# Optimization experiments

Measured on AMD Instinct MI355X. Metric: run time of the kernel, lower is better.

Reference implementation:

```python
import jax, jax.numpy as jnp
import numpy as np

N_E = 1024
E_DIM = 256
GAMMA = 0.1
TEMPERATURE = 0.1


def setup_inputs() -> dict:
    key = jax.random.key(0)
    k1, k2 = jax.random.split(key)
    z = jax.random.normal(k1, (64, 512, E_DIM), dtype=jnp.float32)
    # embedding initialized uniform(-1/n_e, 1/n_e) as in the torch module
    emb = jax.random.uniform(k2, (N_E, E_DIM), dtype=jnp.float32,
                             minval=-1.0 / N_E, maxval=1.0 / N_E)
    return {"z": z, "emb": emb}


def reference(z, emb):
    # z: [B, S, D] -> flatten to [N, D]
    zf = z.reshape(-1, E_DIM)
    # squared euclidean distance via sum-of-squares + matmul: [N, n_e]
    d = (jnp.sum(zf * zf, axis=1, keepdims=True)
         + jnp.sum(emb * emb, axis=1)
         - 2.0 * jnp.einsum('nd,ed->ne', zf, emb))
    exp_d = jnp.exp(-d / GAMMA)
    # soft assignment weights (note: softmax of exp(-d/gamma)/temperature,
    # exactly as in the original module)
    w = jax.nn.softmax(exp_d / TEMPERATURE, axis=-1)
    return w
```

## Files before the change

kernel.cpp:

```cpp
#include <hip/hip_runtime.h>

#define NTOK 32768
#define NE   1024
#define DD   256

typedef __attribute__((ext_vector_type(4))) float f32x4;

__global__ __launch_bounds__(256) void prep_norm_kernel(
    const float* __restrict__ emb, float* __restrict__ pmax)
{
    __shared__ float sm[4];
    const int w = threadIdx.x >> 6;
    const int l = threadIdx.x & 63;
    float m = 0.f;
#pragma unroll
    for (int k = 0; k < 4; ++k) {
        const int row = blockIdx.x * 16 + w * 4 + k;
        f32x4 v = *(const f32x4*)(emb + (size_t)row * DD + l * 4);
        float ss = v.x * v.x + v.y * v.y + v.z * v.z + v.w * v.w;
#pragma unroll
        for (int off = 32; off; off >>= 1) ss += __shfl_xor(ss, off, 64);
        m = fmaxf(m, ss);
    }
    if (l == 0) sm[w] = m;
    __syncthreads();
    if (threadIdx.x == 0)
        pmax[blockIdx.x] = fmaxf(fmaxf(sm[0], sm[1]), fmaxf(sm[2], sm[3]));
}

__device__ __attribute__((noinline)) void slow_row(
    const float* __restrict__ emb, float* __restrict__ out,
    int row, float ss, f32x4 v, int l)
{
    const int c0 = l * 16;
    float acc[16];
    float s = 0.f;
#pragma unroll
    for (int ch = 0; ch < 4; ++ch) {
        float dot[4] = {0.f, 0.f, 0.f, 0.f};
        float ene[4] = {0.f, 0.f, 0.f, 0.f};
        for (int d4 = 0; d4 < 64; ++d4) {
            f32x4 zz;
            zz.x = __shfl(v.x, d4); zz.y = __shfl(v.y, d4);
            zz.z = __shfl(v.z, d4); zz.w = __shfl(v.w, d4);
#pragma unroll
            for (int c = 0; c < 4; ++c) {
                f32x4 ev = *(const f32x4*)(emb + (size_t)(c0 + ch * 4 + c) * DD + d4 * 4);
                dot[c] = fmaf(zz.x, ev.x, fmaf(zz.y, ev.y,
                         fmaf(zz.z, ev.z, fmaf(zz.w, ev.w, dot[c]))));
                ene[c] = fmaf(ev.x, ev.x, fmaf(ev.y, ev.y,
                         fmaf(ev.z, ev.z, fmaf(ev.w, ev.w, ene[c]))));
            }
        }
#pragma unroll
        for (int c = 0; c < 4; ++c) {
            const float d = ss + ene[c] - 2.0f * dot[c];
            const float u = 10.0f * expf(-10.0f * d);
            const float e = expf(u);
            acc[ch * 4 + c] = e;
            s += e;
        }
    }
#pragma unroll
    for (int off = 32; off; off >>= 1) s += __shfl_xor(s, off, 64);
    const float inv = 1.0f / s;
#pragma unroll
    for (int ch = 0; ch < 4; ++ch) {
        f32x4 o = { acc[ch * 4] * inv, acc[ch * 4 + 1] * inv,
                    acc[ch * 4 + 2] * inv, acc[ch * 4 + 3] * inv };
        *(f32x4*)(out + (size_t)row * NE + c0 + ch * 4) = o;
    }
}

__global__ __launch_bounds__(256, 8) void sq_main_kernel(
    const float* __restrict__ z, const float* __restrict__ emb,
    const float* __restrict__ pmax, float* __restrict__ out)
{
    const int w  = threadIdx.x >> 6;
    const int l  = threadIdx.x & 63;
    const int r0 = (blockIdx.x * 4 + w) * 2;

    f32x4 v0 = *(const f32x4*)(z + (size_t)r0 * DD + l * 4);
    f32x4 v1 = *(const f32x4*)(z + (size_t)(r0 + 1) * DD + l * 4);

    float m = pmax[l];
#pragma unroll
    for (int off = 32; off; off >>= 1) m = fmaxf(m, __shfl_xor(m, off, 64));
    const float E   = sqrtf(m);
    const float rhs = (3.0f + E) * (3.0f + E);

    float s0 = v0.x * v0.x + v0.y * v0.y + v0.z * v0.z + v0.w * v0.w;
    float s1 = v1.x * v1.x + v1.y * v1.y + v1.z * v1.z + v1.w * v1.w;
#pragma unroll
    for (int off = 32; off; off >>= 1) {
        s0 += __shfl_xor(s0, off, 64);
        s1 += __shfl_xor(s1, off, 64);
    }

    const float c = 0.0009765625f;
    const f32x4 cv = {c, c, c, c};
    if (s0 >= rhs) {
        float* ob = out + (size_t)r0 * NE + l * 4;
#pragma unroll
        for (int i = 0; i < 4; ++i) *(f32x4*)(ob + i * 256) = cv;
    } else {
        slow_row(emb, out, r0, s0, v0, l);
    }
    if (s1 >= rhs) {
        float* ob = out + (size_t)(r0 + 1) * NE + l * 4;
#pragma unroll
        for (int i = 0; i < 4; ++i) *(f32x4*)(ob + i * 256) = cv;
    } else {
        slow_row(emb, out, r0 + 1, s1, v1, l);
    }
}

extern "C" void kernel_launch(void* const* d_in, const int* in_sizes, int n_in,
                              void* d_out, int out_size, void* d_ws, size_t ws_size,
                              hipStream_t stream) {
    (void)in_sizes; (void)n_in; (void)out_size; (void)ws_size;
    const float* z   = (const float*)d_in[0];
    const float* emb = (const float*)d_in[1];
    float* out = (float*)d_out;
    float* pmax = (float*)d_ws;

    hipLaunchKernelGGL(prep_norm_kernel, dim3(64), dim3(256), 0, stream,
                       emb, pmax);
    hipLaunchKernelGGL(sq_main_kernel, dim3(NTOK / 8), dim3(256), 0, stream,
                       z, emb, pmax, out);
}
```

Measured before the change: 35.32 us.

## Precompute per-row skip flags in a separate kernel before output fill

Moves the per-row norm test (z norm against the largest embedding norm) out of the main kernel into a new kernel that writes one byte flag per row. The fill kernel then handles four rows per wave, reads a packed 4-row flag word, and streams the constant uniform output with no z load or reductions when every flag is clear. This removes z reads and shuffle reductions from the write-bound fill path. In exchange it adds a third kernel launch, a serialized pass over z, and a dependency through workspace memory.

```diff
diff --git a/kernel.cpp b/kernel.cpp
--- a/kernel.cpp
+++ b/kernel.cpp
@@ -5,6 +5,7 @@
 #define DD   256
 
 typedef __attribute__((ext_vector_type(4))) float f32x4;
+
 
 __global__ __launch_bounds__(256) void prep_norm_kernel(
     const float* __restrict__ emb, float* __restrict__ pmax)
@@ -26,6 +27,42 @@
     __syncthreads();
     if (threadIdx.x == 0)
         pmax[blockIdx.x] = fmaxf(fmaxf(sm[0], sm[1]), fmaxf(sm[2], sm[3]));
+}
+
+__global__ __launch_bounds__(256) void zflag_kernel(
+    const float* __restrict__ z, const float* __restrict__ pmax,
+    unsigned char* __restrict__ flags)
+{
+    const int w  = threadIdx.x >> 6;
+    const int l  = threadIdx.x & 63;
+    const int r0 = (blockIdx.x * 4 + w) * 4;
+
+    f32x4 v[4];
+#pragma unroll
+    for (int k = 0; k < 4; ++k)
+        v[k] = *(const f32x4*)(z + (size_t)(r0 + k) * DD + l * 4);
+
+    float m = pmax[l];
+#pragma unroll
+    for (int off = 32; off; off >>= 1) m = fmaxf(m, __shfl_xor(m, off, 64));
+    const float E   = sqrtf(m);
+    const float rhs = (3.0f + E) * (3.0f + E);
+
+    float ss[4];
+#pragma unroll
+    for (int k = 0; k < 4; ++k)
+        ss[k] = v[k].x * v[k].x + v[k].y * v[k].y + v[k].z * v[k].z + v[k].w * v[k].w;
+#pragma unroll
+    for (int off = 32; off; off >>= 1)
+#pragma unroll
+        for (int k = 0; k < 4; ++k) ss[k] += __shfl_xor(ss[k], off, 64);
+
+    if (l == 0) {
+        uchar4 f;
+        f.x = ss[0] < rhs; f.y = ss[1] < rhs;
+        f.z = ss[2] < rhs; f.w = ss[3] < rhs;
+        *(uchar4*)(flags + r0) = f;
+    }
 }
 
 __device__ __attribute__((noinline)) void slow_row(
@@ -72,46 +109,38 @@
     }
 }
 
-__global__ __launch_bounds__(256, 8) void sq_main_kernel(
+__global__ __launch_bounds__(256, 8) void fill_kernel(
     const float* __restrict__ z, const float* __restrict__ emb,
-    const float* __restrict__ pmax, float* __restrict__ out)
+    const unsigned char* __restrict__ flags, float* __restrict__ out)
 {
     const int w  = threadIdx.x >> 6;
     const int l  = threadIdx.x & 63;
-    const int r0 = (blockIdx.x * 4 + w) * 2;
+    const int r0 = (blockIdx.x * 4 + w) * 4;
 
-    f32x4 v0 = *(const f32x4*)(z + (size_t)r0 * DD + l * 4);
-    f32x4 v1 = *(const f32x4*)(z + (size_t)(r0 + 1) * DD + l * 4);
-
-    float m = pmax[l];
-#pragma unroll
-    for (int off = 32; off; off >>= 1) m = fmaxf(m, __shfl_xor(m, off, 64));
-    const float E   = sqrtf(m);
-    const float rhs = (3.0f + E) * (3.0f + E);
-
-    float s0 = v0.x * v0.x + v0.y * v0.y + v0.z * v0.z + v0.w * v0.w;
-    float s1 = v1.x * v1.x + v1.y * v1.y + v1.z * v1.z + v1.w * v1.w;
-#pragma unroll
-    for (int off = 32; off; off >>= 1) {
-        s0 += __shfl_xor(s0, off, 64);
-        s1 += __shfl_xor(s1, off, 64);
-    }
-
+    const unsigned f4 = *(const unsigned*)(flags + r0);
     const float c = 0.0009765625f;
     const f32x4 cv = {c, c, c, c};
-    if (s0 >= rhs) {
+
+    if (f4 == 0u) {
         float* ob = out + (size_t)r0 * NE + l * 4;
 #pragma unroll
-        for (int i = 0; i < 4; ++i) *(f32x4*)(ob + i * 256) = cv;
-    } else {
-        slow_row(emb, out, r0, s0, v0, l);
+        for (int i = 0; i < 16; ++i)
+            *(f32x4*)(ob + (size_t)i * 256) = cv;
+        return;
     }
-    if (s1 >= rhs) {
-        float* ob = out + (size_t)(r0 + 1) * NE + l * 4;
 #pragma unroll
-        for (int i = 0; i < 4; ++i) *(f32x4*)(ob + i * 256) = cv;
-    } else {
-        slow_row(emb, out, r0 + 1, s1, v1, l);
+    for (int k = 0; k < 4; ++k) {
+        float* ob = out + (size_t)(r0 + k) * NE + l * 4;
+        if (((f4 >> (k * 8)) & 0xffu) == 0u) {
+#pragma unroll
+            for (int i = 0; i < 4; ++i) *(f32x4*)(ob + i * 256) = cv;
+        } else {
+            f32x4 v = *(const f32x4*)(z + (size_t)(r0 + k) * DD + l * 4);
+            float ss = v.x * v.x + v.y * v.y + v.z * v.z + v.w * v.w;
+#pragma unroll
+            for (int off = 32; off; off >>= 1) ss += __shfl_xor(ss, off, 64);
+            slow_row(emb, out, r0 + k, ss, v, l);
+        }
     }
 }
 
@@ -123,9 +152,12 @@
     const float* emb = (const float*)d_in[1];
     float* out = (float*)d_out;
     float* pmax = (float*)d_ws;
+    unsigned char* flags = (unsigned char*)d_ws + 256;
 
     hipLaunchKernelGGL(prep_norm_kernel, dim3(64), dim3(256), 0, stream,
                        emb, pmax);
-    hipLaunchKernelGGL(sq_main_kernel, dim3(NTOK / 8), dim3(256), 0, stream,
-                       z, emb, pmax, out);
+    hipLaunchKernelGGL(zflag_kernel, dim3(NTOK / 16), dim3(256), 0, stream,
+                       z, pmax, flags);
+    hipLaunchKernelGGL(fill_kernel, dim3(NTOK / 16), dim3(256), 0, stream,
+                       z, emb, flags, out);
 }
```

Result: slower. 36.85 us (+4.3%).
